# Optimization experiments

Hardware: AMD Instinct MI355X
Metric: run time of the kernel (lower is better)

The kernel has to match this reference:

```python
import jax, jax.numpy as jnp
import numpy as np
jax.config.update("jax_enable_x64", True)  # int64 snake sort keys, matching torch

GRID_3D = 1.0
MULT = 100000


def setup_inputs() -> dict:
    rng = np.random.default_rng(0)
    B, N_views, N_lidar, N_img, C = 4, 6, 16384, 4096, 256
    W_img, H_img = 1600.0, 900.0

    lidar_tokens = rng.standard_normal((B, N_lidar, C)).astype(np.float32)
    img_tokens = rng.standard_normal((B, N_img, C)).astype(np.float32)
    lidar_coords = rng.uniform(-50.0, 50.0, (B, N_lidar, 3)).astype(np.float32)

    # intrinsics: fx,fy ~ 1000-1200, principal point at image center
    K = np.zeros((B, N_views, 3, 3), np.float32)
    K[..., 0, 0] = rng.uniform(1000.0, 1200.0, (B, N_views))
    K[..., 1, 1] = rng.uniform(1000.0, 1200.0, (B, N_views))
    K[..., 0, 2] = W_img / 2
    K[..., 1, 2] = H_img / 2
    K[..., 2, 2] = 1.0

    # proper SE(3) camera-to-world poses
    T = np.zeros((B, N_views, 4, 4), np.float32)
    for b in range(B):
        for n in range(N_views):
            Q, _ = np.linalg.qr(rng.standard_normal((3, 3)))
            if np.linalg.det(Q) < 0:
                Q[:, 0] *= -1
            T[b, n, :3, :3] = Q
            T[b, n, :3, 3] = rng.uniform(-10.0, 10.0, 3)
            T[b, n, 3, 3] = 1.0

    post_rots = (np.eye(3, dtype=np.float32)[None, None]
                 + 0.01 * rng.standard_normal((B, N_views, 3, 3)).astype(np.float32))
    post_trans = 0.1 * rng.standard_normal((B, N_views, 3)).astype(np.float32)

    # img_kuvd: [camera_id, u, v, depth]
    cam_ids = rng.integers(0, N_views, (B, N_img)).astype(np.float32)
    u = rng.uniform(0.0, W_img, (B, N_img)).astype(np.float32)
    v = rng.uniform(0.0, H_img, (B, N_img)).astype(np.float32)
    d = rng.uniform(1.0, 60.0, (B, N_img)).astype(np.float32)
    img_kuvd = np.stack([cam_ids, u, v, d], axis=-1)

    return {
        "lidar_tokens": jnp.asarray(lidar_tokens),
        "lidar_coords": jnp.asarray(lidar_coords),
        "img_tokens": jnp.asarray(img_tokens),
        "img_kuvd": jnp.asarray(img_kuvd),
        "K": jnp.asarray(K),
        "T_c2w": jnpp if False else jnp.asarray(T),
        "post_rots": jnp.asarray(post_rots),
        "post_trans": jnp.asarray(post_trans),
        "lidar_padding_mask": jnp.zeros((B, N_lidar), bool),
        "img_padding_mask": jnp.zeros((B, N_img), bool),
    }


def _unproject(img_kuvd, K, T_c2w, post_rots, post_trans):
    # gather per-token camera params via camera index (first channel)
    cam_idx = img_kuvd[..., 0].astype(jnp.int32)          # [B,T]
    gather = lambda P: jax.vmap(lambda Pb, ib: Pb[ib])(P, cam_idx)
    tK, tT = gather(K), gather(T_c2w)                     # [B,T,3,3],[B,T,4,4]
    tR, tt = gather(post_rots), gather(post_trans)        # [B,T,3,3],[B,T,3]
    u, v, D = img_kuvd[..., 1], img_kuvd[..., 2], img_kuvd[..., 3]
    ones = jnp.ones_like(u)[..., None]
    # invert post transform: uv = R^{-1} (uv1 - t)
    uv1 = jnp.concatenate([u[..., None], v[..., None], ones], -1) - tt
    uv = jnp.einsum('btij,btj->bti', jnp.linalg.inv(tR), uv1)[..., :2]
    # unproject: cam = K^{-1} [u,v,1] * D ; world = T_c2w [cam,1]
    uv1 = jnp.concatenate([uv, ones], -1)
    cam = jnp.einsum('btij,btj->bti', jnp.linalg.inv(tK), uv1) * D[..., None]
    homo = jnp.concatenate([cam, ones], -1)
    return jnp.einsum('btij,btj->bti', tT, homo)[..., :3]


def reference(lidar_tokens, lidar_coords, img_tokens, img_kuvd, K, T_c2w,
              post_rots, post_trans, lidar_padding_mask, img_padding_mask):
    # mode='3d'
    img_coords_3d = _unproject(img_kuvd, K, T_c2w, post_rots, post_trans)
    coords = jnp.concatenate([lidar_coords, img_coords_3d], axis=1)   # [B,N,3]
    tokens = jnp.concatenate([lidar_tokens, img_tokens], axis=1)      # [B,N,C]
    mask = jnp.concatenate([lidar_padding_mask, img_padding_mask], axis=1)

    q = jnp.floor(coords / GRID_3D).astype(jnp.int64)
    q = q - q.min(axis=1, keepdims=True)
    d0, d1, d2 = q[:, :, 0], q[:, :, 1], q[:, :, 2]
    max_d1 = d1.max(axis=1, keepdims=True)
    max_d2 = d2.max(axis=1, keepdims=True)
    snake_d1 = jnp.where(d0 % 2 == 1, max_d1 - d1, d1)
    snake_d2 = jnp.where((d0 + d1) % 2 == 1, max_d2 - d2, d2)
    keys = d0 * (MULT * MULT) + snake_d1 * MULT + snake_d2
    keys = jnp.where(mask, jnp.iinfo(jnp.int64).max, keys)

    idx = jnp.argsort(keys, axis=1)                                   # [B,N]
    sorted_tokens = jnp.take_along_axis(tokens, idx[..., None], axis=1)
    sorted_mask = jnp.take_along_axis(mask, idx, axis=1)
    return sorted_tokens, idx, sorted_mask, lidar_tokens.shape[1], 1
```

## Files before the change

kernel.cpp:

```cpp
#include <hip/hip_runtime.h>
#include <stdint.h>

#define NB      4
#define N_LIDAR 16384
#define N_IMG   4096
#define N_TOT   20480
#define N_PAD   32768
#define NC      256
#define NVIEWS  6
#define MULTK   100000LL
#define BLOCKS_PER_B 80

#define TOK_END ((size_t)NB * N_TOT * NC)
#define IDX_END (TOK_END + (size_t)NB * N_TOT)
#define MSK_END (IDX_END + (size_t)NB * N_TOT)

#define WS_COMPS_OFF 0
#define WS_QBUF_OFF  ((size_t)NB * N_PAD * 8)
#define WS_MM_OFF    (WS_QBUF_OFF + (size_t)NB * N_TOT * 16)
#define WS_BMM_OFF   (WS_MM_OFF + 256)

__global__ __launch_bounds__(256) void quant_kernel(
    const float* __restrict__ lidar_coords,
    const float* __restrict__ kuvd,
    const float* __restrict__ Kmat,
    const float* __restrict__ Tmat,
    const float* __restrict__ postR,
    const float* __restrict__ postT,
    int4* __restrict__ qbuf, int* __restrict__ blockmm)
{
    int gid = blockIdx.x * blockDim.x + threadIdx.x;
    int b = gid / N_TOT, i = gid - b * N_TOT;
    int q0, q1, q2;
    if (i < N_LIDAR) {
        const float* c = lidar_coords + ((size_t)b * N_LIDAR + i) * 3;
        q0 = (int)floorf(c[0]);
        q1 = (int)floorf(c[1]);
        q2 = (int)floorf(c[2]);
    } else {
        int ii = i - N_LIDAR;
        const float* kv = kuvd + ((size_t)b * N_IMG + ii) * 4;
        int cam = (int)kv[0];
        double u = kv[1], v = kv[2], D = kv[3];
        const float* R  = postR + ((size_t)b * NVIEWS + cam) * 9;
        const float* t  = postT + ((size_t)b * NVIEWS + cam) * 3;
        const float* Km = Kmat  + ((size_t)b * NVIEWS + cam) * 9;
        const float* T  = Tmat  + ((size_t)b * NVIEWS + cam) * 16;
        double x0 = u - (double)t[0];
        double x1 = v - (double)t[1];
        double x2 = 1.0 - (double)t[2];
        double r00=R[0], r01=R[1], r02=R[2];
        double r10=R[3], r11=R[4], r12=R[5];
        double r20=R[6], r21=R[7], r22=R[8];
        double c00 = r11*r22 - r12*r21;
        double c01 = r02*r21 - r01*r22;
        double c02 = r01*r12 - r02*r11;
        double c10 = r12*r20 - r10*r22;
        double c11 = r00*r22 - r02*r20;
        double c12 = r02*r10 - r00*r12;
        double det = r00*(r11*r22 - r12*r21)
                   - r01*(r10*r22 - r12*r20)
                   + r02*(r10*r21 - r11*r20);
        double inv = 1.0 / det;
        double w0 = (c00*x0 + c01*x1 + c02*x2) * inv;
        double w1 = (c10*x0 + c11*x1 + c12*x2) * inv;
        double fx = Km[0], cx = Km[2], fy = Km[4], cy = Km[5];
        double camx = (w0 - cx) / fx * D;
        double camy = (w1 - cy) / fy * D;
        double camz = D;
        double wx = (double)T[0]*camx + (double)T[1]*camy + (double)T[2]*camz  + (double)T[3];
        double wy = (double)T[4]*camx + (double)T[5]*camy + (double)T[6]*camz  + (double)T[7];
        double wz = (double)T[8]*camx + (double)T[9]*camy + (double)T[10]*camz + (double)T[11];
        q0 = (int)floor(wx);
        q1 = (int)floor(wy);
        q2 = (int)floor(wz);
    }
    qbuf[gid] = make_int4(q0, q1, q2, 0);

    int mn0=q0, mx0=q0, mn1=q1, mx1=q1, mn2=q2, mx2=q2;
    #pragma unroll
    for (int off = 32; off; off >>= 1) {
        mn0 = min(mn0, __shfl_xor(mn0, off));
        mx0 = max(mx0, __shfl_xor(mx0, off));
        mn1 = min(mn1, __shfl_xor(mn1, off));
        mx1 = max(mx1, __shfl_xor(mx1, off));
        mn2 = min(mn2, __shfl_xor(mn2, off));
        mx2 = max(mx2, __shfl_xor(mx2, off));
    }
    __shared__ int sred[4][6];
    int wid = threadIdx.x >> 6;
    if ((threadIdx.x & 63) == 0) {
        sred[wid][0]=mn0; sred[wid][1]=mn1; sred[wid][2]=mn2;
        sred[wid][3]=mx0; sred[wid][4]=mx1; sred[wid][5]=mx2;
    }
    __syncthreads();
    if (threadIdx.x == 0) {
        int v0=sred[0][0], v1=sred[0][1], v2=sred[0][2];
        int v3=sred[0][3], v4=sred[0][4], v5=sred[0][5];
        #pragma unroll
        for (int w = 1; w < 4; ++w) {
            v0=min(v0,sred[w][0]); v1=min(v1,sred[w][1]); v2=min(v2,sred[w][2]);
            v3=max(v3,sred[w][3]); v4=max(v4,sred[w][4]); v5=max(v5,sred[w][5]);
        }
        int* dst = blockmm + blockIdx.x * 6;
        dst[0]=v0; dst[1]=v1; dst[2]=v2; dst[3]=v3; dst[4]=v4; dst[5]=v5;
    }
}

__global__ __launch_bounds__(128) void reduce_mm_kernel(
    const int* __restrict__ blockmm, int* __restrict__ mm)
{
    int b = blockIdx.x;
    int t = threadIdx.x;
    __shared__ int swave[2][6];
    int v[6];
    if (t < BLOCKS_PER_B) {
        const int* src = blockmm + (b * BLOCKS_PER_B + t) * 6;
        #pragma unroll
        for (int c = 0; c < 6; ++c) v[c] = src[c];
    } else {
        v[0]=v[1]=v[2]=0x7FFFFFFF;
        v[3]=v[4]=v[5]=(int)0x80000000;
    }
    #pragma unroll
    for (int off = 32; off; off >>= 1) {
        v[0]=min(v[0],__shfl_xor(v[0],off));
        v[1]=min(v[1],__shfl_xor(v[1],off));
        v[2]=min(v[2],__shfl_xor(v[2],off));
        v[3]=max(v[3],__shfl_xor(v[3],off));
        v[4]=max(v[4],__shfl_xor(v[4],off));
        v[5]=max(v[5],__shfl_xor(v[5],off));
    }
    int wid = t >> 6;
    if ((t & 63) == 0) {
        #pragma unroll
        for (int c = 0; c < 6; ++c) swave[wid][c] = v[c];
    }
    __syncthreads();
    if (t == 0) {
        mm[b*3+0]      = min(swave[0][0], swave[1][0]);
        mm[b*3+1]      = min(swave[0][1], swave[1][1]);
        mm[b*3+2]      = min(swave[0][2], swave[1][2]);
        mm[12 + b*3+0] = max(swave[0][3], swave[1][3]);
        mm[12 + b*3+1] = max(swave[0][4], swave[1][4]);
        mm[12 + b*3+2] = max(swave[0][5], swave[1][5]);
    }
}

__device__ inline unsigned long long make_comp(
    int b, int i, const int4* __restrict__ qbuf, const int* __restrict__ mm,
    const unsigned char* __restrict__ lmask, const unsigned char* __restrict__ imask)
{
    if (i >= N_TOT) return ~0ull;
    int4 q = qbuf[b * N_TOT + i];
    int mn0 = mm[b*3+0], mn1 = mm[b*3+1], mn2 = mm[b*3+2];
    int d0 = q.x - mn0, d1 = q.y - mn1, d2 = q.z - mn2;
    int max1 = mm[12 + b*3+1] - mn1;
    int max2 = mm[12 + b*3+2] - mn2;
    long long s1 = (d0 & 1) ? (long long)(max1 - d1) : (long long)d1;
    long long s2 = ((d0 + d1) & 1) ? (long long)(max2 - d2) : (long long)d2;
    long long key = (long long)d0 * (MULTK * MULTK) + s1 * MULTK + s2;
    bool m = (i < N_LIDAR) ? (lmask[b * N_LIDAR + i] != 0)
                           : (imask[b * N_IMG + (i - N_LIDAR)] != 0);
    if (m) key = (1LL << 45);
    return ((unsigned long long)key << 16) | (unsigned)i;
}

__global__ __launch_bounds__(1024) void sort_local_full_kernel(
    const int4* __restrict__ qbuf, const int* __restrict__ mm,
    const unsigned char* __restrict__ lmask, const unsigned char* __restrict__ imask,
    unsigned long long* __restrict__ comps)
{
    __shared__ unsigned long long smem[4096];
    int blk = blockIdx.x;
    int b = blk >> 3, bb = blk & 7;
    int base = bb * 4096;
    int t = threadIdx.x;
    #pragma unroll
    for (int s = 0; s < 4; ++s) {
        int i = t + s * 1024;
        smem[i] = make_comp(b, base + i, qbuf, mm, lmask, imask);
    }
    __syncthreads();
    for (int k = 2; k <= 4096; k <<= 1) {
        for (int j = k >> 1; j > 0; j >>= 1) {
            #pragma unroll
            for (int pp = 0; pp < 2; ++pp) {
                int p = t + pp * 1024;
                int i = ((p & ~(j-1)) << 1) | (p & (j-1));
                int l = i | j;
                bool up = (((base + i) & k) == 0);
                unsigned long long a = smem[i], c = smem[l];
                if ((a > c) == up) { smem[i] = c; smem[l] = a; }
            }
            __syncthreads();
        }
    }
    unsigned long long* seg = comps + ((size_t)b << 15) + base;
    #pragma unroll
    for (int s = 0; s < 4; ++s) { int i = t + s*1024; seg[i] = smem[i]; }
}

__global__ __launch_bounds__(1024) void sort_local_merge_kernel(
    unsigned long long* __restrict__ comps, int k)
{
    __shared__ unsigned long long smem[4096];
    int blk = blockIdx.x;
    int b = blk >> 3, bb = blk & 7;
    int base = bb * 4096;
    int t = threadIdx.x;
    unsigned long long* seg = comps + ((size_t)b << 15) + base;
    #pragma unroll
    for (int s = 0; s < 4; ++s) { int i = t + s*1024; smem[i] = seg[i]; }
    __syncthreads();
    for (int j = 2048; j > 0; j >>= 1) {
        #pragma unroll
        for (int pp = 0; pp < 2; ++pp) {
            int p = t + pp * 1024;
            int i = ((p & ~(j-1)) << 1) | (p & (j-1));
            int l = i | j;
            bool up = (((base + i) & k) == 0);
            unsigned long long a = smem[i], c = smem[l];
            if ((a > c) == up) { smem[i] = c; smem[l] = a; }
        }
        __syncthreads();
    }
    #pragma unroll
    for (int s = 0; s < 4; ++s) { int i = t + s*1024; seg[i] = smem[i]; }
}

template<int JM, int K>
__device__ inline void phase_step(unsigned long long (&e)[8], int low) {
    #pragma unroll
    for (int m = 0; m < 8; ++m) {
        if ((m & JM) == 0) {
            int p = m | JM;
            int i_idx = low + (m << 12);
            bool up = ((i_idx & K) == 0);
            unsigned long long a = e[m], c = e[p];
            if ((a > c) == up) { e[m] = c; e[p] = a; }
        }
    }
}

template<int K>
__global__ __launch_bounds__(256) void sort_phase_global_kernel(
    unsigned long long* __restrict__ comps)
{
    int gid = blockIdx.x * blockDim.x + threadIdx.x;
    int b = gid >> 12, low = gid & 4095;
    unsigned long long* seg = comps + ((size_t)b << 15);
    unsigned long long e[8];
    #pragma unroll
    for (int m = 0; m < 8; ++m) e[m] = seg[low + (m << 12)];
    if constexpr (K >= 32768) phase_step<4, K>(e, low);
    if constexpr (K >= 16384) phase_step<2, K>(e, low);
    phase_step<1, K>(e, low);
    #pragma unroll
    for (int m = 0; m < 8; ++m) seg[low + (m << 12)] = e[m];
}

__global__ __launch_bounds__(256) void gather_kernel(
    const unsigned long long* __restrict__ comps,
    const float* __restrict__ lidar_tokens,
    const float* __restrict__ img_tokens,
    const unsigned char* __restrict__ lmask,
    const unsigned char* __restrict__ imask,
    float* __restrict__ out)
{
    int row  = blockIdx.x * 4 + (threadIdx.x >> 6);
    int lane = threadIdx.x & 63;
    int b = row / N_TOT, pos = row - b * N_TOT;
    unsigned long long comp = comps[((size_t)b << 15) + pos];
    int src = (int)(comp & 0xFFFFu);
    const float4* srcp;
    if (src < N_LIDAR)
        srcp = (const float4*)(lidar_tokens + ((size_t)b * N_LIDAR + src) * NC);
    else
        srcp = (const float4*)(img_tokens + ((size_t)b * N_IMG + (src - N_LIDAR)) * NC);
    float4* dstp = (float4*)(out + (size_t)row * NC);
    dstp[lane] = srcp[lane];
    if (lane == 0) {
        out[TOK_END + row] = (float)src;
        bool m = (src < N_LIDAR) ? (lmask[b * N_LIDAR + src] != 0)
                                 : (imask[b * N_IMG + (src - N_LIDAR)] != 0);
        out[IDX_END + row] = m ? 1.0f : 0.0f;
        if (row == 0) {
            out[MSK_END]     = (float)N_LIDAR;
            out[MSK_END + 1] = 1.0f;
        }
    }
}

extern "C" void kernel_launch(void* const* d_in, const int* in_sizes, int n_in,
                              void* d_out, int out_size, void* d_ws, size_t ws_size,
                              hipStream_t stream) {
    const float* lidar_tokens = (const float*)d_in[0];
    const float* lidar_coords = (const float*)d_in[1];
    const float* img_tokens   = (const float*)d_in[2];
    const float* img_kuvd     = (const float*)d_in[3];
    const float* Kmat         = (const float*)d_in[4];
    const float* Tmat         = (const float*)d_in[5];
    const float* postR        = (const float*)d_in[6];
    const float* postT        = (const float*)d_in[7];
    const unsigned char* lmask = (const unsigned char*)d_in[8];
    const unsigned char* imask = (const unsigned char*)d_in[9];
    float* out = (float*)d_out;

    char* ws = (char*)d_ws;
    unsigned long long* comps = (unsigned long long*)(ws + WS_COMPS_OFF);
    int4* qbuf    = (int4*)(ws + WS_QBUF_OFF);
    int*  mm      = (int*)(ws + WS_MM_OFF);
    int*  blockmm = (int*)(ws + WS_BMM_OFF);

    quant_kernel<<<(NB * N_TOT) / 256, 256, 0, stream>>>(
        lidar_coords, img_kuvd, Kmat, Tmat, postR, postT, qbuf, blockmm);
    reduce_mm_kernel<<<NB, 128, 0, stream>>>(blockmm, mm);

    sort_local_full_kernel<<<32, 1024, 0, stream>>>(qbuf, mm, lmask, imask, comps);

    const int PBLK = (NB * 4096) / 256;
    sort_phase_global_kernel<8192><<<PBLK, 256, 0, stream>>>(comps);
    sort_local_merge_kernel<<<32, 1024, 0, stream>>>(comps, 8192);
    sort_phase_global_kernel<16384><<<PBLK, 256, 0, stream>>>(comps);
    sort_local_merge_kernel<<<32, 1024, 0, stream>>>(comps, 16384);
    sort_phase_global_kernel<32768><<<PBLK, 256, 0, stream>>>(comps);
    sort_local_merge_kernel<<<32, 1024, 0, stream>>>(comps, 32768);

    gather_kernel<<<(NB * N_TOT) / 4, 256, 0, stream>>>(
        comps, lidar_tokens, img_tokens, lmask, imask, out);
}
```

Measured before the change: 244.2 us.

## Fuse min/max reduce and global bitonic phases into block-local merge kernels

Drops the separate min/max reduction kernel and recomputes the per-batch reduction inside the local sort kernel. Each global bitonic phase plus its following local merge becomes one kernel. Every block loads the C strided elements it needs, does the cross-block compare-exchanges redundantly in registers, keeps its own slice, and finishes the merge in shared memory, ping-ponging between two buffers. The gather now handles 8 rows per wave, reading all 8 source rows before writing any of them to raise memory-level parallelism. Together this removes four kernel launches and the global round-trips between phases, at the cost of redundant global reads and compare work in the fused kernels.

```diff
diff --git a/kernel.cpp b/kernel.cpp
--- a/kernel.cpp
+++ b/kernel.cpp
@@ -15,10 +15,10 @@
 #define IDX_END (TOK_END + (size_t)NB * N_TOT)
 #define MSK_END (IDX_END + (size_t)NB * N_TOT)
 
-#define WS_COMPS_OFF 0
-#define WS_QBUF_OFF  ((size_t)NB * N_PAD * 8)
-#define WS_MM_OFF    (WS_QBUF_OFF + (size_t)NB * N_TOT * 16)
-#define WS_BMM_OFF   (WS_MM_OFF + 256)
+#define WS_COMPSA_OFF 0
+#define WS_QBUF_OFF   ((size_t)NB * N_PAD * 8)
+#define WS_COMPSB_OFF WS_QBUF_OFF
+#define WS_BMM_OFF    (WS_QBUF_OFF + (size_t)NB * N_TOT * 16)
 
 __global__ __launch_bounds__(256) void quant_kernel(
     const float* __restrict__ lidar_coords,
@@ -107,56 +107,14 @@
     }
 }
 
-__global__ __launch_bounds__(128) void reduce_mm_kernel(
-    const int* __restrict__ blockmm, int* __restrict__ mm)
-{
-    int b = blockIdx.x;
-    int t = threadIdx.x;
-    __shared__ int swave[2][6];
-    int v[6];
-    if (t < BLOCKS_PER_B) {
-        const int* src = blockmm + (b * BLOCKS_PER_B + t) * 6;
-        #pragma unroll
-        for (int c = 0; c < 6; ++c) v[c] = src[c];
-    } else {
-        v[0]=v[1]=v[2]=0x7FFFFFFF;
-        v[3]=v[4]=v[5]=(int)0x80000000;
-    }
-    #pragma unroll
-    for (int off = 32; off; off >>= 1) {
-        v[0]=min(v[0],__shfl_xor(v[0],off));
-        v[1]=min(v[1],__shfl_xor(v[1],off));
-        v[2]=min(v[2],__shfl_xor(v[2],off));
-        v[3]=max(v[3],__shfl_xor(v[3],off));
-        v[4]=max(v[4],__shfl_xor(v[4],off));
-        v[5]=max(v[5],__shfl_xor(v[5],off));
-    }
-    int wid = t >> 6;
-    if ((t & 63) == 0) {
-        #pragma unroll
-        for (int c = 0; c < 6; ++c) swave[wid][c] = v[c];
-    }
-    __syncthreads();
-    if (t == 0) {
-        mm[b*3+0]      = min(swave[0][0], swave[1][0]);
-        mm[b*3+1]      = min(swave[0][1], swave[1][1]);
-        mm[b*3+2]      = min(swave[0][2], swave[1][2]);
-        mm[12 + b*3+0] = max(swave[0][3], swave[1][3]);
-        mm[12 + b*3+1] = max(swave[0][4], swave[1][4]);
-        mm[12 + b*3+2] = max(swave[0][5], swave[1][5]);
-    }
-}
-
-__device__ inline unsigned long long make_comp(
-    int b, int i, const int4* __restrict__ qbuf, const int* __restrict__ mm,
+__device__ inline unsigned long long make_comp2(
+    int b, int i, const int4* __restrict__ qbuf,
+    int mn0, int mn1, int mn2, int max1, int max2,
     const unsigned char* __restrict__ lmask, const unsigned char* __restrict__ imask)
 {
     if (i >= N_TOT) return ~0ull;
     int4 q = qbuf[b * N_TOT + i];
-    int mn0 = mm[b*3+0], mn1 = mm[b*3+1], mn2 = mm[b*3+2];
     int d0 = q.x - mn0, d1 = q.y - mn1, d2 = q.z - mn2;
-    int max1 = mm[12 + b*3+1] - mn1;
-    int max2 = mm[12 + b*3+2] - mn2;
     long long s1 = (d0 & 1) ? (long long)(max1 - d1) : (long long)d1;
     long long s2 = ((d0 + d1) & 1) ? (long long)(max2 - d2) : (long long)d2;
     long long key = (long long)d0 * (MULTK * MULTK) + s1 * MULTK + s2;
@@ -167,19 +125,45 @@
 }
 
 __global__ __launch_bounds__(1024) void sort_local_full_kernel(
-    const int4* __restrict__ qbuf, const int* __restrict__ mm,
+    const int4* __restrict__ qbuf, const int* __restrict__ blockmm,
     const unsigned char* __restrict__ lmask, const unsigned char* __restrict__ imask,
     unsigned long long* __restrict__ comps)
 {
     __shared__ unsigned long long smem[4096];
+    __shared__ int smm[6];
     int blk = blockIdx.x;
     int b = blk >> 3, bb = blk & 7;
     int base = bb * 4096;
     int t = threadIdx.x;
+
+    if (t < 64) {
+        const int* src = blockmm + (b * BLOCKS_PER_B + t) * 6;
+        int v0 = src[0], v1 = src[1], v2 = src[2];
+        int v3 = src[3], v4 = src[4], v5 = src[5];
+        if (t < BLOCKS_PER_B - 64) {
+            const int* s2 = blockmm + (b * BLOCKS_PER_B + 64 + t) * 6;
+            v0 = min(v0, s2[0]); v1 = min(v1, s2[1]); v2 = min(v2, s2[2]);
+            v3 = max(v3, s2[3]); v4 = max(v4, s2[4]); v5 = max(v5, s2[5]);
+        }
+        #pragma unroll
+        for (int off = 32; off; off >>= 1) {
+            v0 = min(v0, __shfl_xor(v0, off));
+            v1 = min(v1, __shfl_xor(v1, off));
+            v2 = min(v2, __shfl_xor(v2, off));
+            v3 = max(v3, __shfl_xor(v3, off));
+            v4 = max(v4, __shfl_xor(v4, off));
+            v5 = max(v5, __shfl_xor(v5, off));
+        }
+        if (t == 0) { smm[0]=v0; smm[1]=v1; smm[2]=v2; smm[3]=v3; smm[4]=v4; smm[5]=v5; }
+    }
+    __syncthreads();
+    int mn0 = smm[0], mn1 = smm[1], mn2 = smm[2];
+    int max1 = smm[4] - mn1, max2 = smm[5] - mn2;
+
     #pragma unroll
     for (int s = 0; s < 4; ++s) {
         int i = t + s * 1024;
-        smem[i] = make_comp(b, base + i, qbuf, mm, lmask, imask);
+        smem[i] = make_comp2(b, base + i, qbuf, mn0, mn1, mn2, max1, max2, lmask, imask);
     }
     __syncthreads();
     for (int k = 2; k <= 4096; k <<= 1) {
@@ -201,63 +185,55 @@
     for (int s = 0; s < 4; ++s) { int i = t + s*1024; seg[i] = smem[i]; }
 }
 
-__global__ __launch_bounds__(1024) void sort_local_merge_kernel(
-    unsigned long long* __restrict__ comps, int k)
+template<int C>
+__global__ __launch_bounds__(1024) void sort_phase_fused_kernel(
+    const unsigned long long* __restrict__ in, unsigned long long* __restrict__ outc)
 {
     __shared__ unsigned long long smem[4096];
     int blk = blockIdx.x;
     int b = blk >> 3, bb = blk & 7;
-    int base = bb * 4096;
+    const int g0 = bb & ~(C - 1);
+    const int sel = bb & (C - 1);
+    const bool up = ((bb & C) == 0);
+    const unsigned long long* inseg = in + ((size_t)b << 15);
     int t = threadIdx.x;
-    unsigned long long* seg = comps + ((size_t)b << 15) + base;
-    #pragma unroll
-    for (int s = 0; s < 4; ++s) { int i = t + s*1024; smem[i] = seg[i]; }
+    #pragma unroll
+    for (int s = 0; s < 4; ++s) {
+        int low = t + s * 1024;
+        unsigned long long e[C];
+        #pragma unroll
+        for (int mi = 0; mi < C; ++mi)
+            e[mi] = inseg[low + ((g0 + mi) << 12)];
+        #pragma unroll
+        for (int JM = C >> 1; JM > 0; JM >>= 1) {
+            #pragma unroll
+            for (int mi = 0; mi < C; ++mi) {
+                if ((mi & JM) == 0) {
+                    unsigned long long a = e[mi], c2 = e[mi | JM];
+                    if ((a > c2) == up) { e[mi] = c2; e[mi | JM] = a; }
+                }
+            }
+        }
+        unsigned long long keep = e[0];
+        #pragma unroll
+        for (int mi = 1; mi < C; ++mi) if (sel == mi) keep = e[mi];
+        smem[low] = keep;
+    }
     __syncthreads();
     for (int j = 2048; j > 0; j >>= 1) {
         #pragma unroll
         for (int pp = 0; pp < 2; ++pp) {
             int p = t + pp * 1024;
-            int i = ((p & ~(j-1)) << 1) | (p & (j-1));
+            int i = ((p & ~(j - 1)) << 1) | (p & (j - 1));
             int l = i | j;
-            bool up = (((base + i) & k) == 0);
-            unsigned long long a = smem[i], c = smem[l];
-            if ((a > c) == up) { smem[i] = c; smem[l] = a; }
+            unsigned long long a = smem[i], c2 = smem[l];
+            if ((a > c2) == up) { smem[i] = c2; smem[l] = a; }
         }
         __syncthreads();
     }
-    #pragma unroll
-    for (int s = 0; s < 4; ++s) { int i = t + s*1024; seg[i] = smem[i]; }
-}
-
-template<int JM, int K>
-__device__ inline void phase_step(unsigned long long (&e)[8], int low) {
-    #pragma unroll
-    for (int m = 0; m < 8; ++m) {
-        if ((m & JM) == 0) {
-            int p = m | JM;
-            int i_idx = low + (m << 12);
-            bool up = ((i_idx & K) == 0);
-            unsigned long long a = e[m], c = e[p];
-            if ((a > c) == up) { e[m] = c; e[p] = a; }
-        }
-    }
-}
-
-template<int K>
-__global__ __launch_bounds__(256) void sort_phase_global_kernel(
-    unsigned long long* __restrict__ comps)
-{
-    int gid = blockIdx.x * blockDim.x + threadIdx.x;
-    int b = gid >> 12, low = gid & 4095;
-    unsigned long long* seg = comps + ((size_t)b << 15);
-    unsigned long long e[8];
-    #pragma unroll
-    for (int m = 0; m < 8; ++m) e[m] = seg[low + (m << 12)];
-    if constexpr (K >= 32768) phase_step<4, K>(e, low);
-    if constexpr (K >= 16384) phase_step<2, K>(e, low);
-    phase_step<1, K>(e, low);
-    #pragma unroll
-    for (int m = 0; m < 8; ++m) seg[low + (m << 12)] = e[m];
+    unsigned long long* outseg = outc + ((size_t)b << 15) + bb * 4096;
+    #pragma unroll
+    for (int s = 0; s < 4; ++s) { int i = t + s * 1024; outseg[i] = smem[i]; }
 }
 
 __global__ __launch_bounds__(256) void gather_kernel(
@@ -268,27 +244,38 @@
     const unsigned char* __restrict__ imask,
     float* __restrict__ out)
 {
-    int row  = blockIdx.x * 4 + (threadIdx.x >> 6);
-    int lane = threadIdx.x & 63;
-    int b = row / N_TOT, pos = row - b * N_TOT;
-    unsigned long long comp = comps[((size_t)b << 15) + pos];
-    int src = (int)(comp & 0xFFFFu);
-    const float4* srcp;
-    if (src < N_LIDAR)
-        srcp = (const float4*)(lidar_tokens + ((size_t)b * N_LIDAR + src) * NC);
-    else
-        srcp = (const float4*)(img_tokens + ((size_t)b * N_IMG + (src - N_LIDAR)) * NC);
-    float4* dstp = (float4*)(out + (size_t)row * NC);
-    dstp[lane] = srcp[lane];
-    if (lane == 0) {
-        out[TOK_END + row] = (float)src;
-        bool m = (src < N_LIDAR) ? (lmask[b * N_LIDAR + src] != 0)
-                                 : (imask[b * N_IMG + (src - N_LIDAR)] != 0);
+    int wave = threadIdx.x >> 6, lane = threadIdx.x & 63;
+    int row0 = (blockIdx.x * 4 + wave) * 8;
+    int b = row0 / N_TOT;
+    int pos0 = row0 - b * N_TOT;
+    unsigned long long carr = comps[((size_t)b << 15) + pos0 + (lane & 7)];
+    int srcs[8];
+    #pragma unroll
+    for (int r = 0; r < 8; ++r)
+        srcs[r] = (int)(__shfl(carr, r) & 0xFFFFu);
+    float4 vals[8];
+    #pragma unroll
+    for (int r = 0; r < 8; ++r) {
+        int s = srcs[r];
+        const float4* p = (s < N_LIDAR)
+            ? (const float4*)(lidar_tokens + ((size_t)b * N_LIDAR + s) * NC)
+            : (const float4*)(img_tokens + ((size_t)b * N_IMG + (s - N_LIDAR)) * NC);
+        vals[r] = p[lane];
+    }
+    #pragma unroll
+    for (int r = 0; r < 8; ++r)
+        ((float4*)(out + (size_t)(row0 + r) * NC))[lane] = vals[r];
+    if (lane < 8) {
+        int s = (int)(carr & 0xFFFFu);
+        int row = row0 + lane;
+        out[TOK_END + row] = (float)s;
+        bool m = (s < N_LIDAR) ? (lmask[b * N_LIDAR + s] != 0)
+                               : (imask[b * N_IMG + s - N_LIDAR] != 0);
         out[IDX_END + row] = m ? 1.0f : 0.0f;
-        if (row == 0) {
-            out[MSK_END]     = (float)N_LIDAR;
-            out[MSK_END + 1] = 1.0f;
-        }
+    }
+    if (row0 == 0 && lane == 0) {
+        out[MSK_END]     = (float)N_LIDAR;
+        out[MSK_END + 1] = 1.0f;
     }
 }
 
@@ -308,25 +295,20 @@
     float* out = (float*)d_out;
 
     char* ws = (char*)d_ws;
-    unsigned long long* comps = (unsigned long long*)(ws + WS_COMPS_OFF);
+    unsigned long long* compsA = (unsigned long long*)(ws + WS_COMPSA_OFF);
+    unsigned long long* compsB = (unsigned long long*)(ws + WS_COMPSB_OFF);
     int4* qbuf    = (int4*)(ws + WS_QBUF_OFF);
-    int*  mm      = (int*)(ws + WS_MM_OFF);
     int*  blockmm = (int*)(ws + WS_BMM_OFF);
 
     quant_kernel<<<(NB * N_TOT) / 256, 256, 0, stream>>>(
         lidar_coords, img_kuvd, Kmat, Tmat, postR, postT, qbuf, blockmm);
-    reduce_mm_kernel<<<NB, 128, 0, stream>>>(blockmm, mm);
-
-    sort_local_full_kernel<<<32, 1024, 0, stream>>>(qbuf, mm, lmask, imask, comps);
-
-    const int PBLK = (NB * 4096) / 256;
-    sort_phase_global_kernel<8192><<<PBLK, 256, 0, stream>>>(comps);
-    sort_local_merge_kernel<<<32, 1024, 0, stream>>>(comps, 8192);
-    sort_phase_global_kernel<16384><<<PBLK, 256, 0, stream>>>(comps);
-    sort_local_merge_kernel<<<32, 1024, 0, stream>>>(comps, 16384);
-    sort_phase_global_kernel<32768><<<PBLK, 256, 0, stream>>>(comps);
-    sort_local_merge_kernel<<<32, 1024, 0, stream>>>(comps, 32768);
-
-    gather_kernel<<<(NB * N_TOT) / 4, 256, 0, stream>>>(
-        comps, lidar_tokens, img_tokens, lmask, imask, out);
-}
+
+    sort_local_full_kernel<<<32, 1024, 0, stream>>>(qbuf, blockmm, lmask, imask, compsA);
+
+    sort_phase_fused_kernel<2><<<32, 1024, 0, stream>>>(compsA, compsB);
+    sort_phase_fused_kernel<4><<<32, 1024, 0, stream>>>(compsB, compsA);
+    sort_phase_fused_kernel<8><<<32, 1024, 0, stream>>>(compsA, compsB);
+
+    gather_kernel<<<(NB * N_TOT) / 32, 256, 0, stream>>>(
+        compsB, lidar_tokens, img_tokens, lmask, imask, out);
+}
```

New measurement: 241.6 us. About the same (-1.1%).
